# Performance work log

Measured on AMD Instinct MI355X. Metric: run time of the kernel, lower is better.

## Reference

```python
import jax, jax.numpy as jnp
import numpy as np

B, T, D_IN, H, D_OUT = 4096, 512, 10, 20, 2


def setup_inputs() -> dict:
    key = jax.random.key(0)
    ks = jax.random.split(key, 12)
    s = 1.0 / np.sqrt(H)  # PyTorch-style uniform bound scale (use normal*s)
    return {
        "x": jax.random.normal(ks[0], (B, T, D_IN), jnp.float32),
        "w_ih0": jax.random.normal(ks[1], (H, D_IN), jnp.float32) * s,
        "w_hh0": jax.random.normal(ks[2], (H, H), jnp.float32) * s,
        "b_ih0": jax.random.normal(ks[3], (H,), jnp.float32) * s,
        "b_hh0": jax.random.normal(ks[4], (H,), jnp.float32) * s,
        "w_ih1": jax.random.normal(ks[5], (H, H), jnp.float32) * s,
        "w_hh1": jax.random.normal(ks[6], (H, H), jnp.float32) * s,
        "b_ih1": jax.random.normal(ks[7], (H,), jnp.float32) * s,
        "b_hh1": jax.random.normal(ks[8], (H,), jnp.float32) * s,
        "fc_w": jax.random.normal(ks[9], (D_OUT, H), jnp.float32) * s,
        "fc_b": jax.random.normal(ks[10], (D_OUT,), jnp.float32) * s,
    }


def _rnn_layer(inp, w_ih, w_hh, b_ih, b_hh):
    # inp: [B, T, Din]. Precompute input projection once (batched GEMM),
    # then scan the sequential recurrence: h_t = tanh(x_t W_ih^T + b_ih + h_{t-1} W_hh^T + b_hh)
    xp = jnp.einsum('btd,hd->bth', inp, w_ih) + (b_ih + b_hh)  # [B, T, H]

    def step(h, xt):
        h = jnp.tanh(xt + h @ w_hh.T)
        return h, h

    h0 = jnp.zeros((inp.shape[0], w_hh.shape[0]), inp.dtype)
    _, hs = jax.lax.scan(step, h0, jnp.swapaxes(xp, 0, 1))  # hs: [T, B, H]
    return jnp.swapaxes(hs, 0, 1)  # [B, T, H]


def reference(x, w_ih0, w_hh0, b_ih0, b_hh0, w_ih1, w_hh1, b_ih1, b_hh1, fc_w, fc_b):
    h1 = _rnn_layer(x, w_ih0, w_hh0, b_ih0, b_hh0)
    h2 = _rnn_layer(h1, w_ih1, w_hh1, b_ih1, b_hh1)
    last = h2[:, -1, :]  # [B, H]
    return last @ fc_w.T + fc_b  # [B, D_OUT]
```

## Files before the change

kernel.cpp:

```cpp
#include <hip/hip_runtime.h>
#include <cstdint>

constexpr int B_   = 4096;
constexpr int T_   = 512;
constexpr int DIN  = 10;
constexpr int H_   = 20;
constexpr int DOUT = 2;

constexpr int SPW = 3;
constexpr int CH  = 4;
constexpr int XV  = CH * DIN / 4;

typedef float v2f __attribute__((ext_vector_type(2)));
typedef float v4f __attribute__((ext_vector_type(4)));

#define CFENCE() asm volatile("" ::: "memory")

__device__ __forceinline__ v2f pkfma(v2f a, v2f b, v2f c) {
    return __builtin_elementwise_fma(a, b, c);
}
__device__ __forceinline__ v2f lohalf(v4f v) { return __builtin_shufflevector(v, v, 0, 1); }
__device__ __forceinline__ v2f hihalf(v4f v) { return __builtin_shufflevector(v, v, 2, 3); }

__device__ __forceinline__ float fast_tanh(float v) {
    float e = __builtin_amdgcn_exp2f(v * 2.885390082f);
    float r = __builtin_amdgcn_rcpf(e + 1.0f);
    return fmaf(-2.0f, r, 1.0f);
}

extern "C" __global__ void __launch_bounds__(64, 1)
rnn_pk(const float* __restrict__ x,
       const float* __restrict__ w_ih0, const float* __restrict__ w_hh0,
       const float* __restrict__ b_ih0, const float* __restrict__ b_hh0,
       const float* __restrict__ w_ih1, const float* __restrict__ w_hh1,
       const float* __restrict__ b_ih1, const float* __restrict__ b_hh1,
       const float* __restrict__ fc_w, const float* __restrict__ fc_b,
       float* __restrict__ out)
{
    const int lane = threadIdx.x;
    const int sl   = lane / H_;
    const int i    = lane - sl * H_;
    const int samp = blockIdx.x * SPW + sl;
    const int sc   = (samp < B_) ? samp : (B_ - 1);
    const int slc  = (sl < SPW) ? sl : SPW;

    __shared__ __align__(16) float h1s[SPW + 1][H_];
    __shared__ __align__(16) float h2s[SPW + 1][H_];

    v2f wi0p[DIN / 2];
    {
        const v2f* p = reinterpret_cast<const v2f*>(w_ih0 + i * DIN);
        #pragma unroll
        for (int k = 0; k < DIN / 2; ++k) wi0p[k] = p[k];
    }
    v2f wh0p[H_ / 2], wi1p[H_ / 2], wh1p[H_ / 2];
    {
        const v4f* p0 = reinterpret_cast<const v4f*>(w_hh0 + i * H_);
        const v4f* p1 = reinterpret_cast<const v4f*>(w_ih1 + i * H_);
        const v4f* p2 = reinterpret_cast<const v4f*>(w_hh1 + i * H_);
        #pragma unroll
        for (int k = 0; k < H_ / 4; ++k) {
            v4f a = p0[k]; wh0p[2*k] = lohalf(a); wh0p[2*k+1] = hihalf(a);
            v4f b = p1[k]; wi1p[2*k] = lohalf(b); wi1p[2*k+1] = hihalf(b);
            v4f c = p2[k]; wh1p[2*k] = lohalf(c); wh1p[2*k+1] = hihalf(c);
        }
    }
    const float bias0 = b_ih0[i] + b_hh0[i];
    const float bias1 = b_ih1[i] + b_hh1[i];

    v2f h1p[H_ / 2], h2p[H_ / 2];
    #pragma unroll
    for (int k = 0; k < H_ / 2; ++k) {
        h1p[k] = (v2f){0.f, 0.f};
        h2p[k] = (v2f){0.f, 0.f};
    }

    const v4f* xb = reinterpret_cast<const v4f*>(x + (size_t)sc * (T_ * DIN));

    v4f xv[XV];
    #pragma unroll
    for (int k = 0; k < XV; ++k) xv[k] = xb[k];

    auto getpair = [&](int p) -> v2f {
        v4f v = xv[p >> 1];
        return (p & 1) ? hihalf(v) : lohalf(v);
    };

    auto full_step = [&](float xpm) {
        v2f aE = (v2f){xpm, 0.f}, aO = (v2f){0.f, 0.f};
        #pragma unroll
        for (int k = 0; k < H_ / 2; k += 2) {
            aE = pkfma(h1p[k],     wh0p[k],     aE);
            aO = pkfma(h1p[k + 1], wh0p[k + 1], aO);
        }
        v2f as = aE + aO;
        float h1n = fast_tanh(as.x + as.y);
        CFENCE();
        h1s[slc][i] = h1n;
        CFENCE();

        v2f bE = (v2f){bias1, 0.f}, bO = (v2f){0.f, 0.f};
        #pragma unroll
        for (int k = 0; k < H_ / 2; k += 2) {
            bE = pkfma(h1p[k],     wi1p[k],     bE);
            bO = pkfma(h1p[k + 1], wi1p[k + 1], bO);
        }
        #pragma unroll
        for (int k = 0; k < H_ / 2; k += 2) {
            bE = pkfma(h2p[k],     wh1p[k],     bE);
            bO = pkfma(h2p[k + 1], wh1p[k + 1], bO);
        }
        v2f bs = bE + bO;
        float h2n = fast_tanh(bs.x + bs.y);
        CFENCE();
        h2s[slc][i] = h2n;
        CFENCE();

        #pragma unroll
        for (int k = 0; k < H_ / 4; ++k) {
            v4f v = reinterpret_cast<const v4f*>(&h1s[slc][0])[k];
            h1p[2*k] = lohalf(v); h1p[2*k+1] = hihalf(v);
        }
        #pragma unroll
        for (int k = 0; k < H_ / 4; ++k) {
            v4f v = reinterpret_cast<const v4f*>(&h2s[slc][0])[k];
            h2p[2*k] = lohalf(v); h2p[2*k+1] = hihalf(v);
        }
        CFENCE();
    };

    auto consume_xp = [&](float (&xp)[CH]) {
        #pragma unroll
        for (int m = 0; m < CH; ++m) {
            v2f acc = (v2f){bias0, 0.f};
            #pragma unroll
            for (int q = 0; q < DIN / 2; ++q)
                acc = pkfma(getpair(m * (DIN / 2) + q), wi0p[q], acc);
            xp[m] = acc.x + acc.y;
        }
    };

    {
        float xp[CH];
        consume_xp(xp);
        #pragma unroll
        for (int k = 0; k < XV; ++k) xv[k] = xb[(CH * DIN) / 4 + k];

        float h1n = fast_tanh(xp[0]);
        CFENCE();
        h1s[slc][i] = h1n;
        CFENCE();
        #pragma unroll
        for (int k = 0; k < H_ / 4; ++k) {
            v4f v = reinterpret_cast<const v4f*>(&h1s[slc][0])[k];
            h1p[2*k] = lohalf(v); h1p[2*k+1] = hihalf(v);
        }
        CFENCE();

        #pragma unroll
        for (int m = 1; m < CH; ++m) full_step(xp[m]);
    }

    for (int t0 = CH; t0 < T_; t0 += CH) {
        float xp[CH];
        consume_xp(xp);
        {
            const int t0n = (t0 + CH < T_) ? (t0 + CH) : 0;
            #pragma unroll
            for (int k = 0; k < XV; ++k) xv[k] = xb[(t0n * DIN) / 4 + k];
        }
        #pragma unroll
        for (int m = 0; m < CH; ++m) full_step(xp[m]);
    }

    {
        v2f bE = (v2f){bias1, 0.f}, bO = (v2f){0.f, 0.f};
        #pragma unroll
        for (int k = 0; k < H_ / 2; k += 2) {
            bE = pkfma(h1p[k],     wi1p[k],     bE);
            bO = pkfma(h1p[k + 1], wi1p[k + 1], bO);
        }
        #pragma unroll
        for (int k = 0; k < H_ / 2; k += 2) {
            bE = pkfma(h2p[k],     wh1p[k],     bE);
            bO = pkfma(h2p[k + 1], wh1p[k + 1], bO);
        }
        v2f bs = bE + bO;
        float h2n = fast_tanh(bs.x + bs.y);
        CFENCE();
        h2s[slc][i] = h2n;
        CFENCE();
        #pragma unroll
        for (int k = 0; k < H_ / 4; ++k) {
            v4f v = reinterpret_cast<const v4f*>(&h2s[slc][0])[k];
            h2p[2*k] = lohalf(v); h2p[2*k+1] = hihalf(v);
        }
        CFENCE();
    }

    if (sl < SPW && samp < B_ && i < DOUT) {
        const v2f* fw = reinterpret_cast<const v2f*>(fc_w + i * H_);
        v2f acc = (v2f){fc_b[i], 0.f};
        #pragma unroll
        for (int k = 0; k < H_ / 2; ++k) acc = pkfma(h2p[k], fw[k], acc);
        out[samp * DOUT + i] = acc.x + acc.y;
    }
}

extern "C" void kernel_launch(void* const* d_in, const int* in_sizes, int n_in,
                              void* d_out, int out_size, void* d_ws, size_t ws_size,
                              hipStream_t stream) {
    (void)in_sizes; (void)n_in; (void)d_ws; (void)ws_size; (void)out_size;
    const float* x     = (const float*)d_in[0];
    const float* w_ih0 = (const float*)d_in[1];
    const float* w_hh0 = (const float*)d_in[2];
    const float* b_ih0 = (const float*)d_in[3];
    const float* b_hh0 = (const float*)d_in[4];
    const float* w_ih1 = (const float*)d_in[5];
    const float* w_hh1 = (const float*)d_in[6];
    const float* b_ih1 = (const float*)d_in[7];
    const float* b_hh1 = (const float*)d_in[8];
    const float* fc_w  = (const float*)d_in[9];
    const float* fc_b  = (const float*)d_in[10];
    float* out = (float*)d_out;

    const int grid = (B_ + SPW - 1) / SPW;
    hipLaunchKernelGGL(rnn_pk, dim3(grid), dim3(64), 0, stream,
                       x, w_ih0, w_hh0, b_ih0, b_hh0,
                       w_ih1, w_hh1, b_ih1, b_hh1, fc_w, fc_b, out);
}
```

Baseline: 144.3 us.

## Broadcast layer-1 hidden state via ds_bpermute and unskew layer schedule

Replaces the shared-memory round trip for the layer-1 hidden state with per-element ds_bpermute broadcasts within each sample's lane group. It drops the one-step skew between the two layers so h2 is computed from the freshly broadcast h1 in the same step. Layer-0 and layer-1 input dot products use scalar FMAs with four accumulators, and the x chunk size is halved. This lengthens the serial dependency chain per step and adds 20 permute instructions, in exchange for removing LDS writes, reads and prologue/epilogue code.

```diff
diff --git a/kernel.cpp b/kernel.cpp
--- a/kernel.cpp
+++ b/kernel.cpp
@@ -8,7 +8,7 @@
 constexpr int DOUT = 2;
 
 constexpr int SPW = 3;
-constexpr int CH  = 4;
+constexpr int CH  = 2;
 constexpr int XV  = CH * DIN / 4;
 
 typedef float v2f __attribute__((ext_vector_type(2)));
@@ -29,7 +29,7 @@
 }
 
 extern "C" __global__ void __launch_bounds__(64, 1)
-rnn_pk(const float* __restrict__ x,
+rnn_bp(const float* __restrict__ x,
        const float* __restrict__ w_ih0, const float* __restrict__ w_hh0,
        const float* __restrict__ b_ih0, const float* __restrict__ b_hh0,
        const float* __restrict__ w_ih1, const float* __restrict__ w_hh1,
@@ -43,8 +43,8 @@
     const int samp = blockIdx.x * SPW + sl;
     const int sc   = (samp < B_) ? samp : (B_ - 1);
     const int slc  = (sl < SPW) ? sl : SPW;
+    const int gb   = ((sl < SPW) ? sl : 0) * H_ * 4;
 
-    __shared__ __align__(16) float h1s[SPW + 1][H_];
     __shared__ __align__(16) float h2s[SPW + 1][H_];
 
     v2f wi0p[DIN / 2];
@@ -53,27 +53,28 @@
         #pragma unroll
         for (int k = 0; k < DIN / 2; ++k) wi0p[k] = p[k];
     }
-    v2f wh0p[H_ / 2], wi1p[H_ / 2], wh1p[H_ / 2];
+    float wh0[H_], wi1[H_];
+    v2f wh1p[H_ / 2];
     {
         const v4f* p0 = reinterpret_cast<const v4f*>(w_hh0 + i * H_);
         const v4f* p1 = reinterpret_cast<const v4f*>(w_ih1 + i * H_);
         const v4f* p2 = reinterpret_cast<const v4f*>(w_hh1 + i * H_);
         #pragma unroll
         for (int k = 0; k < H_ / 4; ++k) {
-            v4f a = p0[k]; wh0p[2*k] = lohalf(a); wh0p[2*k+1] = hihalf(a);
-            v4f b = p1[k]; wi1p[2*k] = lohalf(b); wi1p[2*k+1] = hihalf(b);
+            v4f a = p0[k]; wh0[4*k]=a.x; wh0[4*k+1]=a.y; wh0[4*k+2]=a.z; wh0[4*k+3]=a.w;
+            v4f b = p1[k]; wi1[4*k]=b.x; wi1[4*k+1]=b.y; wi1[4*k+2]=b.z; wi1[4*k+3]=b.w;
             v4f c = p2[k]; wh1p[2*k] = lohalf(c); wh1p[2*k+1] = hihalf(c);
         }
     }
     const float bias0 = b_ih0[i] + b_hh0[i];
     const float bias1 = b_ih1[i] + b_hh1[i];
 
-    v2f h1p[H_ / 2], h2p[H_ / 2];
+    float h1g[H_];
+    v4f   h2q[H_ / 4];
     #pragma unroll
-    for (int k = 0; k < H_ / 2; ++k) {
-        h1p[k] = (v2f){0.f, 0.f};
-        h2p[k] = (v2f){0.f, 0.f};
-    }
+    for (int j = 0; j < H_; ++j) h1g[j] = 0.0f;
+    #pragma unroll
+    for (int k = 0; k < H_ / 4; ++k) h2q[k] = (v4f){0.f, 0.f, 0.f, 0.f};
 
     const v4f* xb = reinterpret_cast<const v4f*>(x + (size_t)sc * (T_ * DIN));
 
@@ -84,49 +85,6 @@
     auto getpair = [&](int p) -> v2f {
         v4f v = xv[p >> 1];
         return (p & 1) ? hihalf(v) : lohalf(v);
-    };
-
-    auto full_step = [&](float xpm) {
-        v2f aE = (v2f){xpm, 0.f}, aO = (v2f){0.f, 0.f};
-        #pragma unroll
-        for (int k = 0; k < H_ / 2; k += 2) {
-            aE = pkfma(h1p[k],     wh0p[k],     aE);
-            aO = pkfma(h1p[k + 1], wh0p[k + 1], aO);
-        }
-        v2f as = aE + aO;
-        float h1n = fast_tanh(as.x + as.y);
-        CFENCE();
-        h1s[slc][i] = h1n;
-        CFENCE();
-
-        v2f bE = (v2f){bias1, 0.f}, bO = (v2f){0.f, 0.f};
-        #pragma unroll
-        for (int k = 0; k < H_ / 2; k += 2) {
-            bE = pkfma(h1p[k],     wi1p[k],     bE);
-            bO = pkfma(h1p[k + 1], wi1p[k + 1], bO);
-        }
-        #pragma unroll
-        for (int k = 0; k < H_ / 2; k += 2) {
-            bE = pkfma(h2p[k],     wh1p[k],     bE);
-            bO = pkfma(h2p[k + 1], wh1p[k + 1], bO);
-        }
-        v2f bs = bE + bO;
-        float h2n = fast_tanh(bs.x + bs.y);
-        CFENCE();
-        h2s[slc][i] = h2n;
-        CFENCE();
-
-        #pragma unroll
-        for (int k = 0; k < H_ / 4; ++k) {
-            v4f v = reinterpret_cast<const v4f*>(&h1s[slc][0])[k];
-            h1p[2*k] = lohalf(v); h1p[2*k+1] = hihalf(v);
-        }
-        #pragma unroll
-        for (int k = 0; k < H_ / 4; ++k) {
-            v4f v = reinterpret_cast<const v4f*>(&h2s[slc][0])[k];
-            h2p[2*k] = lohalf(v); h2p[2*k+1] = hihalf(v);
-        }
-        CFENCE();
     };
 
     auto consume_xp = [&](float (&xp)[CH]) {
@@ -140,28 +98,49 @@
         }
     };
 
-    {
-        float xp[CH];
-        consume_xp(xp);
+    auto full_step = [&](float xpm) {
+        float a0 = xpm, a1 = 0.f, a2 = 0.f, a3 = 0.f;
         #pragma unroll
-        for (int k = 0; k < XV; ++k) xv[k] = xb[(CH * DIN) / 4 + k];
+        for (int j = 0; j < H_; j += 4) {
+            a0 = fmaf(h1g[j+0], wh0[j+0], a0);
+            a1 = fmaf(h1g[j+1], wh0[j+1], a1);
+            a2 = fmaf(h1g[j+2], wh0[j+2], a2);
+            a3 = fmaf(h1g[j+3], wh0[j+3], a3);
+        }
+        float h1n = fast_tanh((a0 + a1) + (a2 + a3));
 
-        float h1n = fast_tanh(xp[0]);
+        const int h1i = __float_as_int(h1n);
+        #pragma unroll
+        for (int j = 0; j < H_; ++j)
+            h1g[j] = __int_as_float(__builtin_amdgcn_ds_bpermute(gb + 4 * j, h1i));
+
+        float b0 = bias1, b1 = 0.f, b2 = 0.f, b3 = 0.f;
+        #pragma unroll
+        for (int j = 0; j < H_; j += 4) {
+            b0 = fmaf(h1g[j+0], wi1[j+0], b0);
+            b1 = fmaf(h1g[j+1], wi1[j+1], b1);
+            b2 = fmaf(h1g[j+2], wi1[j+2], b2);
+            b3 = fmaf(h1g[j+3], wi1[j+3], b3);
+        }
+        v2f bp0 = (v2f){0.f, 0.f}, bp1 = (v2f){0.f, 0.f};
+        #pragma unroll
+        for (int k = 0; k < H_ / 4; ++k) {
+            bp0 = pkfma(lohalf(h2q[k]), wh1p[2*k],   bp0);
+            bp1 = pkfma(hihalf(h2q[k]), wh1p[2*k+1], bp1);
+        }
+        v2f bs = bp0 + bp1;
+        float h2n = fast_tanh(((b0 + b1) + (b2 + b3)) + (bs.x + bs.y));
+
         CFENCE();
-        h1s[slc][i] = h1n;
+        h2s[slc][i] = h2n;
         CFENCE();
         #pragma unroll
-        for (int k = 0; k < H_ / 4; ++k) {
-            v4f v = reinterpret_cast<const v4f*>(&h1s[slc][0])[k];
-            h1p[2*k] = lohalf(v); h1p[2*k+1] = hihalf(v);
-        }
+        for (int k = 0; k < H_ / 4; ++k)
+            h2q[k] = reinterpret_cast<const v4f*>(&h2s[slc][0])[k];
         CFENCE();
+    };
 
-        #pragma unroll
-        for (int m = 1; m < CH; ++m) full_step(xp[m]);
-    }
-
-    for (int t0 = CH; t0 < T_; t0 += CH) {
+    for (int t0 = 0; t0 < T_; t0 += CH) {
         float xp[CH];
         consume_xp(xp);
         {
@@ -173,36 +152,14 @@
         for (int m = 0; m < CH; ++m) full_step(xp[m]);
     }
 
-    {
-        v2f bE = (v2f){bias1, 0.f}, bO = (v2f){0.f, 0.f};
-        #pragma unroll
-        for (int k = 0; k < H_ / 2; k += 2) {
-            bE = pkfma(h1p[k],     wi1p[k],     bE);
-            bO = pkfma(h1p[k + 1], wi1p[k + 1], bO);
-        }
-        #pragma unroll
-        for (int k = 0; k < H_ / 2; k += 2) {
-            bE = pkfma(h2p[k],     wh1p[k],     bE);
-            bO = pkfma(h2p[k + 1], wh1p[k + 1], bO);
-        }
-        v2f bs = bE + bO;
-        float h2n = fast_tanh(bs.x + bs.y);
-        CFENCE();
-        h2s[slc][i] = h2n;
-        CFENCE();
-        #pragma unroll
-        for (int k = 0; k < H_ / 4; ++k) {
-            v4f v = reinterpret_cast<const v4f*>(&h2s[slc][0])[k];
-            h2p[2*k] = lohalf(v); h2p[2*k+1] = hihalf(v);
-        }
-        CFENCE();
-    }
-
     if (sl < SPW && samp < B_ && i < DOUT) {
         const v2f* fw = reinterpret_cast<const v2f*>(fc_w + i * H_);
         v2f acc = (v2f){fc_b[i], 0.f};
         #pragma unroll
-        for (int k = 0; k < H_ / 2; ++k) acc = pkfma(h2p[k], fw[k], acc);
+        for (int k = 0; k < H_ / 4; ++k) {
+            acc = pkfma(lohalf(h2q[k]), fw[2*k],   acc);
+            acc = pkfma(hihalf(h2q[k]), fw[2*k+1], acc);
+        }
         out[samp * DOUT + i] = acc.x + acc.y;
     }
 }
@@ -225,7 +182,7 @@
     float* out = (float*)d_out;
 
     const int grid = (B_ + SPW - 1) / SPW;
-    hipLaunchKernelGGL(rnn_pk, dim3(grid), dim3(64), 0, stream,
+    hipLaunchKernelGGL(rnn_bp, dim3(grid), dim3(64), 0, stream,
                        x, w_ih0, w_hh0, b_ih0, b_hh0,
                        w_ih1, w_hh1, b_ih1, b_hh1, fc_w, fc_b, out);
 }
```

Measured after the change: 254.4 us. +76.3%, slower.
